# Optimization experiments

Measured on AMD Instinct MI355X. Metric: run time of the kernel, lower is better.

Reference implementation:

```python
import jax, jax.numpy as jnp
import numpy as np

B, T, D_IN, H, L, OUT, S = 128, 256, 8, 512, 2, 2, 32
A = H  # attention_size == hidden_size


def lstm_cell(h, c, xt, Wih, Whh, b):
    # PyTorch LSTM gate order: i, f, g, o ; b = b_ih + b_hh (combined)
    g = xt @ Wih.T + h @ Whh.T + b
    i, f, gg, o = jnp.split(g, 4, axis=-1)
    c = jax.nn.sigmoid(f) * c + jax.nn.sigmoid(i) * jnp.tanh(gg)
    h = jax.nn.sigmoid(o) * jnp.tanh(c)
    return h, c


def setup_inputs() -> dict:
    key = jax.random.key(0)
    ks = jax.random.split(key, 20)
    w = lambda k, shape: jax.random.normal(k, shape, jnp.float32) * 0.1
    return {
        "x": jax.random.normal(ks[0], (B, T, D_IN), jnp.float32),
        # bidirectional encoder, 2 layers; leading dim 2 = (fwd, bwd)
        "enc_Wih0": w(ks[1], (2, 4 * H, D_IN)),
        "enc_Whh0": w(ks[2], (2, 4 * H, H)),
        "enc_b0": w(ks[3], (2, 4 * H)),
        "enc_Wih1": w(ks[4], (2, 4 * H, 2 * H)),
        "enc_Whh1": w(ks[5], (2, 4 * H, H)),
        "enc_b1": w(ks[6], (2, 4 * H)),
        # unidirectional decoder, 2 layers; layer0 input = output_size + 2H
        "dec_Wih0": w(ks[7], (4 * H, 2 * H + OUT)),
        "dec_Whh0": w(ks[8], (4 * H, H)),
        "dec_b0": w(ks[9], (4 * H,)),
        "dec_Wih1": w(ks[10], (4 * H, H)),
        "dec_Whh1": w(ks[11], (4 * H, H)),
        "dec_b1": w(ks[12], (4 * H,)),
        # Bahdanau attention (no biases)
        "Wa": w(ks[13], (A, 2 * H)),
        "Ua": w(ks[14], (A, H)),
        "Va": w(ks[15], (1, A)),
        "proj_W": w(ks[16], (H, H)),
        "proj_b": jnp.zeros((H,), jnp.float32),
        "fc_W": w(ks[17], (OUT, H)),
        "fc_b": jnp.zeros((OUT,), jnp.float32),
    }


def _forward(x, enc_Wih0, enc_Whh0, enc_b0, enc_Wih1, enc_Whh1, enc_b1,
             dec_Wih0, dec_Whh0, dec_b0, dec_Wih1, dec_Whh1, dec_b1,
             Wa, Ua, Va, proj_W, proj_b, fc_W, fc_b):
    Bb = x.shape[0]
    xT = jnp.swapaxes(x, 0, 1)  # [T,B,D]

    def run_dir(seq, Wih, Whh, b, reverse):
        h0 = jnp.zeros((Bb, H), x.dtype)
        def step(carry, xt):
            h, c = lstm_cell(carry[0], carry[1], xt, Wih, Whh, b)
            return (h, c), h
        (hT, cT), hs = jax.lax.scan(step, (h0, h0), seq, reverse=reverse)
        return hs, hT, cT

    # encoder layer 0 (bidirectional)
    of, hf0, cf0 = run_dir(xT, enc_Wih0[0], enc_Whh0[0], enc_b0[0], False)
    ob, hb0, cb0 = run_dir(xT, enc_Wih0[1], enc_Whh0[1], enc_b0[1], True)
    l1in = jnp.concatenate([of, ob], -1)  # [T,B,2H]
    # encoder layer 1
    of1, hf1, cf1 = run_dir(l1in, enc_Wih1[0], enc_Whh1[0], enc_b1[0], False)
    ob1, hb1, cb1 = run_dir(l1in, enc_Wih1[1], enc_Whh1[1], enc_b1[1], True)
    enc_out = jnp.swapaxes(jnp.concatenate([of1, ob1], -1), 0, 1)  # [B,T,2H]

    # torch hidden order: [l0_fwd, l0_bwd, l1_fwd, l1_bwd]; code takes first num_layers=2
    dh = jnp.tanh(jnp.stack([hf0, hb0]) @ proj_W.T + proj_b)  # [2,B,H]
    dc = jnp.stack([cf0, cb0])

    Wa_vals = enc_out @ Wa.T  # [B,T,A], loop-invariant part of attention
    y0 = x[:, -1, :OUT]

    def dec_step(carry, _):
        h, c, y = carry
        q = h[-1]  # [B,H] last-layer hidden
        score = jnp.tanh(Wa_vals + (q @ Ua.T)[:, None, :]) @ Va.T  # [B,T,1]
        wts = jax.nn.softmax(score, axis=1)
        z = jnp.sum(wts * enc_out, axis=1)  # [B,2H]
        h0n, c0n = lstm_cell(h[0], c[0], jnp.concatenate([y, z], 1), dec_Wih0, dec_Whh0, dec_b0)
        h1n, c1n = lstm_cell(h[1], c[1], h0n, dec_Wih1, dec_Whh1, dec_b1)
        yn = h1n @ fc_W.T + fc_b  # [B,OUT]
        return (jnp.stack([h0n, h1n]), jnp.stack([c0n, c1n]), yn), yn

    _, ys = jax.lax.scan(dec_step, (dh, dc, y0), None, length=S)
    return jnp.swapaxes(ys, 0, 1)  # [B,S,OUT]


def reference(x, enc_Wih0, enc_Whh0, enc_b0, enc_Wih1, enc_Whh1, enc_b1,
              dec_Wih0, dec_Whh0, dec_b0, dec_Wih1, dec_Whh1, dec_b1,
              Wa, Ua, Va, proj_W, proj_b, fc_W, fc_b):
    return _forward(x, enc_Wih0, enc_Whh0, enc_b0, enc_Wih1, enc_Whh1, enc_b1,
                    dec_Wih0, dec_Whh0, dec_b0, dec_Wih1, dec_Whh1, dec_b1,
                    Wa, Ua, Va, proj_W, proj_b, fc_W, fc_b)
```

## Files before the change

kernel.cpp:

```cpp
#include <hip/hip_runtime.h>

typedef _Float16 h16;
typedef __attribute__((ext_vector_type(8))) _Float16 f16x8;
typedef __attribute__((ext_vector_type(4))) float f32x4;
typedef unsigned long long u64;
typedef unsigned int u32;
typedef unsigned short u16;

#define B_ 128
#define T_ 256
#define H_ 512
#define S_ 32
#define MFMA __builtin_amdgcn_mfma_f32_16x16x32_f16

__device__ __forceinline__ float fexp2(float x){ return __builtin_amdgcn_exp2f(x); }
__device__ __forceinline__ float frcp (float x){ return __builtin_amdgcn_rcpf(x); }
__device__ __forceinline__ float fsig (float x){ return frcp(1.f + fexp2(-1.44269504089f*x)); }
__device__ __forceinline__ float ftanh(float x){ return 1.f - 2.f*frcp(1.f + fexp2(2.88539008178f*x)); }

__device__ __forceinline__ f16x8 ld16_coh(const h16* p) {
  u64 q0 = __hip_atomic_load((const u64*)p,     __ATOMIC_RELAXED, __HIP_MEMORY_SCOPE_AGENT);
  u64 q1 = __hip_atomic_load((const u64*)p + 1, __ATOMIC_RELAXED, __HIP_MEMORY_SCOPE_AGENT);
  u64 a[2] = {q0, q1};
  f16x8 v; __builtin_memcpy(&v, a, 16);
  return v;
}
__device__ __forceinline__ float ld4f_coh(const float* p) {
  u32 b = __hip_atomic_load((const u32*)p, __ATOMIC_RELAXED, __HIP_MEMORY_SCOPE_AGENT);
  float v; __builtin_memcpy(&v, &b, 4);
  return v;
}
__device__ __forceinline__ float ld2h_coh(const h16* p) {
  u16 b = __hip_atomic_load((const u16*)p, __ATOMIC_RELAXED, __HIP_MEMORY_SCOPE_AGENT);
  h16 v; __builtin_memcpy(&v, &b, 2);
  return (float)v;
}
__device__ __forceinline__ void st2_coh(h16* p, h16 v) {
  u16 b; __builtin_memcpy(&b, &v, 2);
  __hip_atomic_store((u16*)p, b, __ATOMIC_RELAXED, __HIP_MEMORY_SCOPE_AGENT);
}
__device__ __forceinline__ void st4_coh(float* p, float v) {
  u32 b; __builtin_memcpy(&b, &v, 4);
  __hip_atomic_store((u32*)p, b, __ATOMIC_RELAXED, __HIP_MEMORY_SCOPE_AGENT);
}

__device__ __forceinline__ void gridbar(u32* slots, int myslot, int base,
                                        int n, u32 ep, int tid) {
  __syncthreads();
  if (tid == 0)
    __hip_atomic_store(&slots[(size_t)myslot * 32], ep, __ATOMIC_RELAXED, __HIP_MEMORY_SCOPE_AGENT);
  bool ok;
  do {
    ok = (tid < n) ? (__hip_atomic_load(&slots[(size_t)(base + tid) * 32],
                                        __ATOMIC_RELAXED, __HIP_MEMORY_SCOPE_AGENT) >= ep)
                   : true;
  } while (!__syncthreads_and(ok));
  __syncthreads();
}

struct EncP {
  const h16 *xpad, *Wih0, *Whh0, *Wih1, *Whh1;
  const float *b0, *b1;
  h16 *l1in, *encout;
  float *cdump;
  u32* slots;
};

__global__ __launch_bounds__(512, 1) void encoder_persist(EncP P) {
  const int wg = blockIdx.x, dir = wg >> 7;
  const int j0 = (wg & 127) << 2;
  const int tid = threadIdx.x, wid = tid >> 6, lane = tid & 63;
  const int col = lane & 15, rowg = lane >> 4;
  const int u = col & 3, gt = col >> 2;
  const int m0 = wid << 4;

  __shared__ h16 W[16][1544];

  auto stage = [&](const h16* Wih, int Kx, const h16* Whh) {
    const int CX = Kx >> 3, CT = CX + 64;
    for (int i = tid; i < 16 * CT; i += 512) {
      const int r = i / CT, c = i - r * CT;
      const int grow = (r >> 2) * 512 + j0 + (r & 3);
      f16x8 v = (c < CX) ? *(const f16x8*)(Wih + (size_t)grow * Kx + (c << 3))
                         : *(const f16x8*)(Whh + (size_t)grow * 512 + ((c - CX) << 3));
      *(f16x8*)(&W[r][c << 3]) = v;
    }
  };
  auto pick = [&](float own, float p4, float p8, float p12, int x) {
    return x == 0 ? own : x == 1 ? p4 : x == 2 ? p8 : p12;
  };

  u32 ep = 0;
  float c0_ = 0.f, c1_ = 0.f, c2_ = 0.f, c3_ = 0.f;
  float h0, h1, h2, h3;

#define GATECOMB(av_, cvar, hvar, bias_)                                        \
  { float a_ = av_ + bias_;                                                     \
    float p4_ = __shfl_xor(a_, 4), p8_ = __shfl_xor(a_, 8), p12_ = __shfl_xor(a_, 12); \
    float iv = pick(a_, p4_, p8_, p12_, gt);                                    \
    float fv = pick(a_, p4_, p8_, p12_, gt ^ 1);                                \
    float gv = pick(a_, p4_, p8_, p12_, gt ^ 2);                                \
    float ov = pick(a_, p4_, p8_, p12_, gt ^ 3);                                \
    cvar = fsig(fv) * cvar + fsig(iv) * ftanh(gv);                              \
    hvar = fsig(ov) * ftanh(cvar); }

  stage(P.Wih0 + (size_t)dir * 2048 * 32, 32, P.Whh0 + (size_t)dir * 2048 * 512);
  const float bias0 = P.b0[dir * 2048 + gt * 512 + j0 + u];
  __syncthreads();

  for (int i = 0; i < 256; ++i) {
    const int t = dir ? 255 - i : i;
    f32x4 acc = {0.f, 0.f, 0.f, 0.f};
    {
      f16x8 av = *(const f16x8*)(P.xpad + ((size_t)(m0 + col) * T_ + t) * 32 + rowg * 8);
      f16x8 bv = *(const f16x8*)(&W[col][rowg * 8]);
      acc = MFMA(av, bv, acc, 0, 0, 0);
    }
    if (i) {
      const int tp = dir ? t + 1 : t - 1;
      const h16* ah = P.l1in + ((size_t)tp * B_ + m0 + col) * 1024 + dir * 512 + rowg * 8;
      #pragma unroll
      for (int ks = 0; ks < 16; ++ks) {
        f16x8 av = ld16_coh(ah + ks * 32);
        f16x8 bv = *(const f16x8*)(&W[col][32 + ks * 32 + rowg * 8]);
        acc = MFMA(av, bv, acc, 0, 0, 0);
      }
    }
    GATECOMB(acc[0], c0_, h0, bias0) GATECOMB(acc[1], c1_, h1, bias0)
    GATECOMB(acc[2], c2_, h2, bias0) GATECOMB(acc[3], c3_, h3, bias0)
    const float hw = (gt == 0) ? h0 : (gt == 1) ? h1 : (gt == 2) ? h2 : h3;
    const int bm = m0 + (rowg << 2) + gt;
    st2_coh(&P.l1in[((size_t)t * B_ + bm) * 1024 + dir * 512 + j0 + u], (h16)hw);
    gridbar(P.slots, wg, dir << 7, 128, ++ep, tid);
  }
  {
    const float cw = (gt == 0) ? c0_ : (gt == 1) ? c1_ : (gt == 2) ? c2_ : c3_;
    const int bm = m0 + (rowg << 2) + gt;
    P.cdump[(size_t)dir * B_ * H_ + (size_t)bm * H_ + j0 + u] = cw;
  }
  gridbar(P.slots, wg, 0, 256, ++ep, tid);

  stage(P.Wih1 + (size_t)dir * 2048 * 1024, 1024, P.Whh1 + (size_t)dir * 2048 * 512);
  const float bias1 = P.b1[dir * 2048 + gt * 512 + j0 + u];
  c0_ = c1_ = c2_ = c3_ = 0.f;
  __syncthreads();

  for (int i = 0; i < 256; ++i) {
    const int t = dir ? 255 - i : i;
    f32x4 acc = {0.f, 0.f, 0.f, 0.f};
    const h16* ax = P.l1in + ((size_t)t * B_ + m0 + col) * 1024 + rowg * 8;
    #pragma unroll
    for (int ks = 0; ks < 32; ++ks) {
      f16x8 av = *(const f16x8*)(ax + ks * 32);
      f16x8 bv = *(const f16x8*)(&W[col][ks * 32 + rowg * 8]);
      acc = MFMA(av, bv, acc, 0, 0, 0);
    }
    if (i) {
      const int tp = dir ? t + 1 : t - 1;
      const h16* ah = P.encout + ((size_t)(m0 + col) * T_ + tp) * 1024 + dir * 512 + rowg * 8;
      #pragma unroll
      for (int ks = 0; ks < 16; ++ks) {
        f16x8 av = ld16_coh(ah + ks * 32);
        f16x8 bv = *(const f16x8*)(&W[col][1024 + ks * 32 + rowg * 8]);
        acc = MFMA(av, bv, acc, 0, 0, 0);
      }
    }
    GATECOMB(acc[0], c0_, h0, bias1) GATECOMB(acc[1], c1_, h1, bias1)
    GATECOMB(acc[2], c2_, h2, bias1) GATECOMB(acc[3], c3_, h3, bias1)
    const float hw = (gt == 0) ? h0 : (gt == 1) ? h1 : (gt == 2) ? h2 : h3;
    const int bm = m0 + (rowg << 2) + gt;
    st2_coh(&P.encout[((size_t)bm * T_ + t) * 1024 + dir * 512 + j0 + u], (h16)hw);
    gridbar(P.slots, wg, dir << 7, 128, ++ep, tid);
  }
#undef GATECOMB
}

struct DecP {
  const h16 *bUa, *WaV, *enc, *bdWih0, *bdWhh0, *bdWih1, *bdWhh1;
  const float *Va, *db0, *db1, *fcW, *fcb, *cdump;
  float *qUa, *score, *out;
  h16 *xcat, *dh0, *dh1;
  u32* slots;
};

__global__ __launch_bounds__(512, 1) void decoder_persist(DecP D) {
  const int wg = blockIdx.x, tid = threadIdx.x;
  const int wid = tid >> 6, lane = tid & 63;
  const int col = lane & 15, rowg = lane >> 4;
  const int gw = wg * 8 + wid;
  const int mt = wg >> 5, ut = wg & 31;
  const int mi = tid >> 4, ji = tid & 15;

  __shared__ h16 Ast[16][1576];
  __shared__ float gtl[4][16][16];
  __shared__ float sred[256], swts[256];

  float c0r = 0.f, c1r = 0.f;
  if (tid < 256) {
    c0r = D.cdump[(size_t)(mt * 16 + mi) * 512 + ut * 16 + ji];
    c1r = D.cdump[(size_t)B_ * H_ + (size_t)(mt * 16 + mi) * 512 + ut * 16 + ji];
  }
  u32 ep = 0;

  for (int s = 0; s < S_; ++s) {
    const int par = s & 1;
    const h16* h1c = D.dh1 + (size_t)par * B_ * H_;
    h16* h1n = D.dh1 + (size_t)(par ^ 1) * B_ * H_;
    const h16* h0c = D.dh0 + (size_t)par * B_ * H_;
    h16* h0n = D.dh0 + (size_t)(par ^ 1) * B_ * H_;

    if (gw < 256) {
      const int qmt = gw >> 5, qnt = gw & 31;
      f32x4 acc = {0, 0, 0, 0};
      const h16* ap = h1c + (size_t)(qmt * 16 + col) * 512 + rowg * 8;
      const h16* bp = D.bUa + (size_t)(qnt * 16 + col) * 512 + rowg * 8;
      #pragma unroll
      for (int kc = 0; kc < 16; ++kc) {
        f16x8 av = ld16_coh(ap + kc * 32);
        f16x8 bv = *(const f16x8*)(bp + kc * 32);
        acc = MFMA(av, bv, acc, 0, 0, 0);
      }
      #pragma unroll
      for (int t2 = 0; t2 < 4; ++t2)
        st4_coh(D.qUa + (size_t)(qmt * 16 + rowg * 4 + t2) * 512 + qnt * 16 + col, acc[t2]);
    } else if (gw < 512 && s > 0) {
      const int idx = gw - 256, m = idx >> 1, o = idx & 1;
      float sum = 0.f;
      #pragma unroll
      for (int i2 = 0; i2 < 8; ++i2) {
        const int k = i2 * 64 + lane;
        sum += ld2h_coh(h1c + (size_t)m * 512 + k) * D.fcW[o * 512 + k];
      }
      #pragma unroll
      for (int o2 = 32; o2; o2 >>= 1) sum += __shfl_xor(sum, o2);
      if (lane == 0) {
        const float y = sum + D.fcb[o];
        D.out[(size_t)m * (S_ * 2) + (s - 1) * 2 + o] = y;
        st2_coh(D.xcat + (size_t)m * 1056 + o, (h16)y);
      }
    }
    gridbar(D.slots, wg, 0, 256, ++ep, tid);

    {
      const int m = gw >> 4, tg = gw & 15;
      float q[8], va[8];
      #pragma unroll
      for (int i2 = 0; i2 < 8; ++i2) {
        q[i2] = ld4f_coh(D.qUa + (size_t)m * 512 + i2 * 64 + lane);
        va[i2] = D.Va[i2 * 64 + lane];
      }
      for (int tt = 0; tt < 16; ++tt) {
        const int t = tg * 16 + tt;
        const h16* wrow = D.WaV + ((size_t)m * 256 + t) * 512;
        float ssum = 0.f;
        #pragma unroll
        for (int i2 = 0; i2 < 8; ++i2)
          ssum += ftanh((float)wrow[i2 * 64 + lane] + q[i2]) * va[i2];
        #pragma unroll
        for (int o2 = 32; o2; o2 >>= 1) ssum += __shfl_xor(ssum, o2);
        if (lane == 0) st4_coh(D.score + (size_t)m * 256 + t, ssum);
      }
    }
    gridbar(D.slots, wg, 0, 256, ++ep, tid);

    if (wg < 128) {
      const int m = wg;
      const float sv = (tid < 256) ? ld4f_coh(D.score + (size_t)m * 256 + tid) : -1e30f;
      if (tid < 256) sred[tid] = sv;
      __syncthreads();
      for (int o2 = 128; o2; o2 >>= 1) { if (tid < o2) sred[tid] = fmaxf(sred[tid], sred[tid + o2]); __syncthreads(); }
      const float mx = sred[0]; __syncthreads();
      const float p = (tid < 256) ? fexp2((sv - mx) * 1.44269504089f) : 0.f;
      if (tid < 256) sred[tid] = p;
      __syncthreads();
      for (int o2 = 128; o2; o2 >>= 1) { if (tid < o2) sred[tid] += sred[tid + o2]; __syncthreads(); }
      if (tid < 256) swts[tid] = p * frcp(sred[0]);
      __syncthreads();
      const h16* erow = D.enc + (size_t)m * 256 * 1024;
      #pragma unroll
      for (int half = 0; half < 2; ++half) {
        const int k = tid + half * 512;
        float a0 = 0, a1 = 0, a2 = 0, a3 = 0;
        for (int t = 0; t < 256; t += 4) {
          a0 += swts[t    ] * (float)erow[(t    ) * 1024 + k];
          a1 += swts[t + 1] * (float)erow[(t + 1) * 1024 + k];
          a2 += swts[t + 2] * (float)erow[(t + 2) * 1024 + k];
          a3 += swts[t + 3] * (float)erow[(t + 3) * 1024 + k];
        }
        st2_coh(D.xcat + (size_t)m * 1056 + 2 + k, (h16)((a0 + a1) + (a2 + a3)));
      }
    }
    gridbar(D.slots, wg, 0, 256, ++ep, tid);

    {
      for (int i2 = tid; i2 < 16 * 196; i2 += 512) {
        const int r = i2 / 196, c = i2 - r * 196;
        f16x8 v = (c < 132) ? ld16_coh(D.xcat + (size_t)(mt * 16 + r) * 1056 + c * 8)
                            : ld16_coh(h0c + (size_t)(mt * 16 + r) * 512 + (c - 132) * 8);
        *(f16x8*)&Ast[r][c * 8] = v;
      }
      __syncthreads();
      if (wid < 4) {
        const int n = wid * 512 + ut * 16 + col;
        f32x4 acc = {0, 0, 0, 0};
        const h16* w1 = D.bdWih0 + (size_t)n * 1056 + rowg * 8;
        const h16* w2 = D.bdWhh0 + (size_t)n * 512 + rowg * 8;
        #pragma unroll
        for (int kc = 0; kc < 33; ++kc) {
          f16x8 av = *(const f16x8*)&Ast[col][kc * 32 + rowg * 8];
          f16x8 bv = *(const f16x8*)(w1 + kc * 32);
          acc = MFMA(av, bv, acc, 0, 0, 0);
        }
        #pragma unroll
        for (int kc = 0; kc < 16; ++kc) {
          f16x8 av = *(const f16x8*)&Ast[col][1056 + kc * 32 + rowg * 8];
          f16x8 bv = *(const f16x8*)(w2 + kc * 32);
          acc = MFMA(av, bv, acc, 0, 0, 0);
        }
        #pragma unroll
        for (int t2 = 0; t2 < 4; ++t2) gtl[wid][rowg * 4 + t2][col] = acc[t2];
      }
      __syncthreads();
      if (tid < 256) {
        const int jj = ut * 16 + ji;
        const float iv = gtl[0][mi][ji] + D.db0[jj];
        const float fv = gtl[1][mi][ji] + D.db0[512 + jj];
        const float gv = gtl[2][mi][ji] + D.db0[1024 + jj];
        const float ov = gtl[3][mi][ji] + D.db0[1536 + jj];
        c0r = fsig(fv) * c0r + fsig(iv) * ftanh(gv);
        st2_coh(h0n + (size_t)(mt * 16 + mi) * 512 + jj, (h16)(fsig(ov) * ftanh(c0r)));
      }
    }
    gridbar(D.slots, wg, 0, 256, ++ep, tid);

    {
      for (int i2 = tid; i2 < 16 * 128; i2 += 512) {
        const int r = i2 >> 7, c = i2 & 127;
        f16x8 v = (c < 64) ? ld16_coh(h0n + (size_t)(mt * 16 + r) * 512 + c * 8)
                           : ld16_coh(h1c + (size_t)(mt * 16 + r) * 512 + (c - 64) * 8);
        *(f16x8*)&Ast[r][c * 8] = v;
      }
      __syncthreads();
      if (wid < 4) {
        const int n = wid * 512 + ut * 16 + col;
        f32x4 acc = {0, 0, 0, 0};
        const h16* w1 = D.bdWih1 + (size_t)n * 512 + rowg * 8;
        const h16* w2 = D.bdWhh1 + (size_t)n * 512 + rowg * 8;
        #pragma unroll
        for (int kc = 0; kc < 16; ++kc) {
          f16x8 av = *(const f16x8*)&Ast[col][kc * 32 + rowg * 8];
          f16x8 bv = *(const f16x8*)(w1 + kc * 32);
          acc = MFMA(av, bv, acc, 0, 0, 0);
        }
        #pragma unroll
        for (int kc = 0; kc < 16; ++kc) {
          f16x8 av = *(const f16x8*)&Ast[col][512 + kc * 32 + rowg * 8];
          f16x8 bv = *(const f16x8*)(w2 + kc * 32);
          acc = MFMA(av, bv, acc, 0, 0, 0);
        }
        #pragma unroll
        for (int t2 = 0; t2 < 4; ++t2) gtl[wid][rowg * 4 + t2][col] = acc[t2];
      }
      __syncthreads();
      if (tid < 256) {
        const int jj = ut * 16 + ji;
        const float iv = gtl[0][mi][ji] + D.db1[jj];
        const float fv = gtl[1][mi][ji] + D.db1[512 + jj];
        const float gv = gtl[2][mi][ji] + D.db1[1024 + jj];
        const float ov = gtl[3][mi][ji] + D.db1[1536 + jj];
        c1r = fsig(fv) * c1r + fsig(iv) * ftanh(gv);
        st2_coh(h1n + (size_t)(mt * 16 + mi) * 512 + jj, (h16)(fsig(ov) * ftanh(c1r)));
      }
    }
    gridbar(D.slots, wg, 0, 256, ++ep, tid);
  }

  if (gw < 256) {
    const int m = gw >> 1, o = gw & 1;
    const h16* h1f = D.dh1;
    float sum = 0.f;
    #pragma unroll
    for (int i2 = 0; i2 < 8; ++i2) {
      const int k = i2 * 64 + lane;
      sum += ld2h_coh(h1f + (size_t)m * 512 + k) * D.fcW[o * 512 + k];
    }
    #pragma unroll
    for (int o2 = 32; o2; o2 >>= 1) sum += __shfl_xor(sum, o2);
    if (lane == 0) D.out[(size_t)m * (S_ * 2) + (S_ - 1) * 2 + o] = sum + D.fcb[o];
  }
}

__global__ __launch_bounds__(256) void gemm_tn(const h16* Am, int lda, const h16* Bm,
                                               const float* bias, void* Cout, int ldc,
                                               int K, int mode) {
  const int wid = threadIdx.x >> 6, lane = threadIdx.x & 63;
  const int r = lane & 15, g = lane >> 4;
  const int m0 = (blockIdx.x * 4 + wid) * 16;
  const int n0 = blockIdx.y * 64;
  f32x4 acc[4] = {{0,0,0,0},{0,0,0,0},{0,0,0,0},{0,0,0,0}};
  const h16* ap = Am + (size_t)(m0 + r) * lda + g * 8;
  const h16* bp = Bm + (size_t)(n0 + r) * K + g * 8;
  for (int k = 0; k < K; k += 32) {
    f16x8 av = *(const f16x8*)(ap + k);
    #pragma unroll
    for (int j = 0; j < 4; ++j) {
      f16x8 bv = *(const f16x8*)(bp + (size_t)j * 16 * K + k);
      acc[j] = MFMA(av, bv, acc[j], 0, 0, 0);
    }
  }
  #pragma unroll
  for (int j = 0; j < 4; ++j) {
    const int n = n0 + j * 16 + r;
    const float badd = bias ? bias[n] : 0.f;
    #pragma unroll
    for (int t = 0; t < 4; ++t) {
      const int m = m0 + g * 4 + t;
      float v = acc[j][t] + badd;
      if (mode == 2) v = ftanh(v);
      if (mode == 0) ((float*)Cout)[(size_t)m * ldc + n] = v;
      else           ((h16*)Cout) [(size_t)m * ldc + n] = (h16)v;
    }
  }
}

__global__ void convert_pad(const float* __restrict__ in, h16* __restrict__ out,
                            int rows, int Kin, int Kout) {
  const size_t i = (size_t)blockIdx.x * 256 + threadIdx.x;
  if (i >= (size_t)rows * Kout) return;
  const int r = (int)(i / Kout), k = (int)(i % Kout);
  out[i] = (k < Kin) ? (h16)in[(size_t)r * Kin + k] : (h16)0.f;
}

__global__ void y0_init(const float* __restrict__ x, h16* __restrict__ xcat) {
  const int tid = threadIdx.x;
  if (tid < 256) {
    const int m = tid >> 1, o = tid & 1;
    xcat[(size_t)m * 1056 + o] = (h16)x[(size_t)(m * T_ + (T_ - 1)) * 8 + o];
  }
}

extern "C" void kernel_launch(void* const* d_in, const int* in_sizes, int n_in,
                              void* d_out, int out_size, void* d_ws, size_t ws_size,
                              hipStream_t stream) {
  const float* x     = (const float*)d_in[0];
  const float* eWih0 = (const float*)d_in[1];
  const float* eWhh0 = (const float*)d_in[2];
  const float* eb0   = (const float*)d_in[3];
  const float* eWih1 = (const float*)d_in[4];
  const float* eWhh1 = (const float*)d_in[5];
  const float* eb1   = (const float*)d_in[6];
  const float* dWih0 = (const float*)d_in[7];
  const float* dWhh0 = (const float*)d_in[8];
  const float* db0   = (const float*)d_in[9];
  const float* dWih1 = (const float*)d_in[10];
  const float* dWhh1 = (const float*)d_in[11];
  const float* db1   = (const float*)d_in[12];
  const float* Wa    = (const float*)d_in[13];
  const float* Ua    = (const float*)d_in[14];
  const float* Va    = (const float*)d_in[15];
  const float* projW = (const float*)d_in[16];
  const float* projb = (const float*)d_in[17];
  const float* fcW   = (const float*)d_in[18];
  const float* fcb   = (const float*)d_in[19];
  float* out = (float*)d_out;

  size_t cur = 0;
  auto alloc = [&](size_t bytes) {
    void* p = (char*)d_ws + cur;
    cur += (bytes + 255) & ~(size_t)255;
    return p;
  };
  h16*  xpad   = (h16*) alloc((size_t)B_ * T_ * 32 * 2);
  h16*  l1in   = (h16*) alloc((size_t)T_ * B_ * 1024 * 2);
  h16*  encout = (h16*) alloc((size_t)B_ * T_ * 1024 * 2);
  h16*  WaV    = (h16*) alloc((size_t)B_ * T_ * H_ * 2);
  float* cdump = (float*)alloc((size_t)2 * B_ * H_ * 4);
  float* score = (float*)alloc((size_t)B_ * T_ * 4);
  float* qUa   = (float*)alloc((size_t)B_ * H_ * 4);
  h16*  xcat   = (h16*) alloc((size_t)B_ * 1056 * 2);
  h16*  dh0    = (h16*) alloc((size_t)2 * B_ * H_ * 2);
  h16*  dh1    = (h16*) alloc((size_t)2 * B_ * H_ * 2);
  u32*  slots  = (u32*) alloc((size_t)2 * 256 * 32 * 4);
  h16*  bWih0  = (h16*) alloc((size_t)2 * 2048 * 32 * 2);
  h16*  bWhh0  = (h16*) alloc((size_t)2 * 2048 * 512 * 2);
  h16*  bWih1  = (h16*) alloc((size_t)2 * 2048 * 1024 * 2);
  h16*  bWhh1  = (h16*) alloc((size_t)2 * 2048 * 512 * 2);
  h16*  bdWih0 = (h16*) alloc((size_t)2048 * 1056 * 2);
  h16*  bdWhh0 = (h16*) alloc((size_t)2048 * 512 * 2);
  h16*  bdWih1 = (h16*) alloc((size_t)2048 * 512 * 2);
  h16*  bdWhh1 = (h16*) alloc((size_t)2048 * 512 * 2);
  h16*  bWa    = (h16*) alloc((size_t)512 * 1024 * 2);
  h16*  bUa    = (h16*) alloc((size_t)512 * 512 * 2);
  h16*  bprojW = (h16*) alloc((size_t)512 * 512 * 2);
  if (cur > ws_size) return;

  (void)hipMemsetAsync(slots, 0, (size_t)2 * 256 * 32 * 4, stream);
  (void)hipMemsetAsync(xcat, 0, (size_t)B_ * 1056 * 2, stream);

  auto conv = [&](const float* in, h16* o, int rows, int kin, int kout) {
    const size_t total = (size_t)rows * kout;
    convert_pad<<<dim3((unsigned)((total + 255) / 256)), dim3(256), 0, stream>>>(in, o, rows, kin, kout);
  };
  conv(x,     xpad,   B_ * T_,  8,    32);
  conv(eWih0, bWih0,  2 * 2048, 8,    32);
  conv(eWhh0, bWhh0,  2 * 2048, 512,  512);
  conv(eWih1, bWih1,  2 * 2048, 1024, 1024);
  conv(eWhh1, bWhh1,  2 * 2048, 512,  512);
  conv(dWih0, bdWih0, 2048,     1026, 1056);
  conv(dWhh0, bdWhh0, 2048,     512,  512);
  conv(dWih1, bdWih1, 2048,     512,  512);
  conv(dWhh1, bdWhh1, 2048,     512,  512);
  conv(Wa,    bWa,    512,      1024, 1024);
  conv(Ua,    bUa,    512,      512,  512);
  conv(projW, bprojW, 512,      512,  512);

  EncP P;
  P.xpad = xpad; P.Wih0 = bWih0; P.Whh0 = bWhh0; P.Wih1 = bWih1; P.Whh1 = bWhh1;
  P.b0 = eb0; P.b1 = eb1; P.l1in = l1in; P.encout = encout; P.cdump = cdump; P.slots = slots;
  encoder_persist<<<dim3(256), dim3(512), 0, stream>>>(P);

  gemm_tn<<<dim3(B_ * T_ / 64, 8), dim3(256), 0, stream>>>(encout, 1024, bWa, nullptr, WaV, 512, 1024, 1);
  gemm_tn<<<dim3(B_ / 64, 8), dim3(256), 0, stream>>>(l1in + (size_t)(T_ - 1) * B_ * 1024, 1024,
                                                      bprojW, projb, dh0, 512, 512, 2);
  gemm_tn<<<dim3(B_ / 64, 8), dim3(256), 0, stream>>>(l1in + 512, 1024,
                                                      bprojW, projb, dh1, 512, 512, 2);
  y0_init<<<dim3(1), dim3(256), 0, stream>>>(x, xcat);

  DecP D;
  D.bUa = bUa; D.WaV = WaV; D.enc = encout;
  D.bdWih0 = bdWih0; D.bdWhh0 = bdWhh0; D.bdWih1 = bdWih1; D.bdWhh1 = bdWhh1;
  D.Va = Va; D.db0 = db0; D.db1 = db1; D.fcW = fcW; D.fcb = fcb; D.cdump = cdump;
  D.qUa = qUa; D.score = score; D.out = out;
  D.xcat = xcat; D.dh0 = dh0; D.dh1 = dh1;
  D.slots = slots + 256 * 32;
  decoder_persist<<<dim3(256), dim3(512), 0, stream>>>(D);
}
```

Baseline: 10.75 ms.

## Replace epoch-slot grid barriers with per-step atomic counters and prefetch input projection

```diff
diff --git a/kernel.cpp b/kernel.cpp
--- a/kernel.cpp
+++ b/kernel.cpp
@@ -13,6 +13,13 @@
 #define S_ 32
 #define MFMA __builtin_amdgcn_mfma_f32_16x16x32_f16
 
+#define SLOT_L0F 0
+#define SLOT_L0B 257
+#define SLOT_ALL 514
+#define SLOT_L1F 515
+#define SLOT_L1B 771
+#define SLOT_DEC 1027
+
 __device__ __forceinline__ float fexp2(float x){ return __builtin_amdgcn_exp2f(x); }
 __device__ __forceinline__ float frcp (float x){ return __builtin_amdgcn_rcpf(x); }
 __device__ __forceinline__ float fsig (float x){ return frcp(1.f + fexp2(-1.44269504089f*x)); }
@@ -44,18 +51,13 @@
   __hip_atomic_store((u32*)p, b, __ATOMIC_RELAXED, __HIP_MEMORY_SCOPE_AGENT);
 }
 
-__device__ __forceinline__ void gridbar(u32* slots, int myslot, int base,
-                                        int n, u32 ep, int tid) {
+__device__ __forceinline__ void bar_arrive(u32* c, int tid) {
   __syncthreads();
-  if (tid == 0)
-    __hip_atomic_store(&slots[(size_t)myslot * 32], ep, __ATOMIC_RELAXED, __HIP_MEMORY_SCOPE_AGENT);
-  bool ok;
-  do {
-    ok = (tid < n) ? (__hip_atomic_load(&slots[(size_t)(base + tid) * 32],
-                                        __ATOMIC_RELAXED, __HIP_MEMORY_SCOPE_AGENT) >= ep)
-                   : true;
-  } while (!__syncthreads_and(ok));
-  __syncthreads();
+  if (tid == 0) atomicAdd(c, 1u);
+}
+__device__ __forceinline__ void bar_wait(const u32* c, u32 n) {
+  while (__hip_atomic_load(c, __ATOMIC_RELAXED, __HIP_MEMORY_SCOPE_AGENT) < n) {}
+  __builtin_amdgcn_sched_barrier(0);
 }
 
 struct EncP {
@@ -63,7 +65,7 @@
   const float *b0, *b1;
   h16 *l1in, *encout;
   float *cdump;
-  u32* slots;
+  u32* cnt;
 };
 
 __global__ __launch_bounds__(512, 1) void encoder_persist(EncP P) {
@@ -89,8 +91,28 @@
   auto pick = [&](float own, float p4, float p8, float p12, int x) {
     return x == 0 ? own : x == 1 ? p4 : x == 2 ? p8 : p12;
   };
-
-  u32 ep = 0;
+  auto xpart0 = [&](int t) -> f32x4 {
+    f32x4 a = {0.f, 0.f, 0.f, 0.f};
+    f16x8 av = *(const f16x8*)(P.xpad + ((size_t)(m0 + col) * T_ + t) * 32 + rowg * 8);
+    f16x8 bv = *(const f16x8*)(&W[col][rowg * 8]);
+    return MFMA(av, bv, a, 0, 0, 0);
+  };
+  auto xpart1 = [&](int t) -> f32x4 {
+    f32x4 a = {0.f, 0.f, 0.f, 0.f};
+    const h16* ax = P.l1in + ((size_t)t * B_ + m0 + col) * 1024 + rowg * 8;
+    #pragma unroll
+    for (int ks = 0; ks < 32; ++ks) {
+      f16x8 av = *(const f16x8*)(ax + ks * 32);
+      f16x8 bv = *(const f16x8*)(&W[col][ks * 32 + rowg * 8]);
+      a = MFMA(av, bv, a, 0, 0, 0);
+    }
+    return a;
+  };
+
+  u32* cL0 = P.cnt + (size_t)(dir ? SLOT_L0B : SLOT_L0F) * 16;
+  u32* cL1 = P.cnt + (size_t)(dir ? SLOT_L1B : SLOT_L1F) * 16;
+  u32* cAll = P.cnt + (size_t)SLOT_ALL * 16;
+
   float c0_ = 0.f, c1_ = 0.f, c2_ = 0.f, c3_ = 0.f;
   float h0, h1, h2, h3;
 
@@ -108,15 +130,12 @@
   const float bias0 = P.b0[dir * 2048 + gt * 512 + j0 + u];
   __syncthreads();
 
+  f32x4 accx = xpart0(dir ? 255 : 0);
   for (int i = 0; i < 256; ++i) {
     const int t = dir ? 255 - i : i;
-    f32x4 acc = {0.f, 0.f, 0.f, 0.f};
-    {
-      f16x8 av = *(const f16x8*)(P.xpad + ((size_t)(m0 + col) * T_ + t) * 32 + rowg * 8);
-      f16x8 bv = *(const f16x8*)(&W[col][rowg * 8]);
-      acc = MFMA(av, bv, acc, 0, 0, 0);
-    }
+    f32x4 acc = accx;
     if (i) {
+      bar_wait(cL0 + (size_t)(i - 1) * 16, 128);
       const int tp = dir ? t + 1 : t - 1;
       const h16* ah = P.l1in + ((size_t)tp * B_ + m0 + col) * 1024 + dir * 512 + rowg * 8;
       #pragma unroll
@@ -131,31 +150,28 @@
     const float hw = (gt == 0) ? h0 : (gt == 1) ? h1 : (gt == 2) ? h2 : h3;
     const int bm = m0 + (rowg << 2) + gt;
     st2_coh(&P.l1in[((size_t)t * B_ + bm) * 1024 + dir * 512 + j0 + u], (h16)hw);
-    gridbar(P.slots, wg, dir << 7, 128, ++ep, tid);
+    bar_arrive(cL0 + (size_t)i * 16, tid);
+    if (i < 255) accx = xpart0(dir ? 254 - i : i + 1);
   }
   {
     const float cw = (gt == 0) ? c0_ : (gt == 1) ? c1_ : (gt == 2) ? c2_ : c3_;
     const int bm = m0 + (rowg << 2) + gt;
     P.cdump[(size_t)dir * B_ * H_ + (size_t)bm * H_ + j0 + u] = cw;
   }
-  gridbar(P.slots, wg, 0, 256, ++ep, tid);
+  bar_arrive(cAll, tid);
+  bar_wait(cAll, 256);
 
   stage(P.Wih1 + (size_t)dir * 2048 * 1024, 1024, P.Whh1 + (size_t)dir * 2048 * 512);
   const float bias1 = P.b1[dir * 2048 + gt * 512 + j0 + u];
   c0_ = c1_ = c2_ = c3_ = 0.f;
   __syncthreads();
 
+  accx = xpart1(dir ? 255 : 0);
   for (int i = 0; i < 256; ++i) {
     const int t = dir ? 255 - i : i;
-    f32x4 acc = {0.f, 0.f, 0.f, 0.f};
-    const h16* ax = P.l1in + ((size_t)t * B_ + m0 + col) * 1024 + rowg * 8;
-    #pragma unroll
-    for (int ks = 0; ks < 32; ++ks) {
-      f16x8 av = *(const f16x8*)(ax + ks * 32);
-      f16x8 bv = *(const f16x8*)(&W[col][ks * 32 + rowg * 8]);
-      acc = MFMA(av, bv, acc, 0, 0, 0);
-    }
+    f32x4 acc = accx;
     if (i) {
+      bar_wait(cL1 + (size_t)(i - 1) * 16, 128);
       const int tp = dir ? t + 1 : t - 1;
       const h16* ah = P.encout + ((size_t)(m0 + col) * T_ + tp) * 1024 + dir * 512 + rowg * 8;
       #pragma unroll
@@ -170,7 +186,8 @@
     const float hw = (gt == 0) ? h0 : (gt == 1) ? h1 : (gt == 2) ? h2 : h3;
     const int bm = m0 + (rowg << 2) + gt;
     st2_coh(&P.encout[((size_t)bm * T_ + t) * 1024 + dir * 512 + j0 + u], (h16)hw);
-    gridbar(P.slots, wg, dir << 7, 128, ++ep, tid);
+    bar_arrive(cL1 + (size_t)i * 16, tid);
+    if (i < 255) accx = xpart1(dir ? 254 - i : i + 1);
   }
 #undef GATECOMB
 }
@@ -180,7 +197,7 @@
   const float *Va, *db0, *db1, *fcW, *fcb, *cdump;
   float *qUa, *score, *out;
   h16 *xcat, *dh0, *dh1;
-  u32* slots;
+  u32* cnt;
 };
 
 __global__ __launch_bounds__(512, 1) void decoder_persist(DecP D) {
@@ -195,12 +212,19 @@
   __shared__ float gtl[4][16][16];
   __shared__ float sred[256], swts[256];
 
+  u32* cD = D.cnt + (size_t)SLOT_DEC * 16;
+  u32 ep = 0;
+  auto dbar = [&]() {
+    bar_arrive(cD + (size_t)ep * 16, tid);
+    bar_wait(cD + (size_t)ep * 16, 256);
+    ++ep;
+  };
+
   float c0r = 0.f, c1r = 0.f;
   if (tid < 256) {
     c0r = D.cdump[(size_t)(mt * 16 + mi) * 512 + ut * 16 + ji];
     c1r = D.cdump[(size_t)B_ * H_ + (size_t)(mt * 16 + mi) * 512 + ut * 16 + ji];
   }
-  u32 ep = 0;
 
   for (int s = 0; s < S_; ++s) {
     const int par = s & 1;
@@ -239,7 +263,7 @@
         st2_coh(D.xcat + (size_t)m * 1056 + o, (h16)y);
       }
     }
-    gridbar(D.slots, wg, 0, 256, ++ep, tid);
+    dbar();
 
     {
       const int m = gw >> 4, tg = gw & 15;
@@ -261,7 +285,7 @@
         if (lane == 0) st4_coh(D.score + (size_t)m * 256 + t, ssum);
       }
     }
-    gridbar(D.slots, wg, 0, 256, ++ep, tid);
+    dbar();
 
     if (wg < 128) {
       const int m = wg;
@@ -290,7 +314,7 @@
         st2_coh(D.xcat + (size_t)m * 1056 + 2 + k, (h16)((a0 + a1) + (a2 + a3)));
       }
     }
-    gridbar(D.slots, wg, 0, 256, ++ep, tid);
+    dbar();
 
     {
       for (int i2 = tid; i2 < 16 * 196; i2 += 512) {
@@ -331,7 +355,7 @@
         st2_coh(h0n + (size_t)(mt * 16 + mi) * 512 + jj, (h16)(fsig(ov) * ftanh(c0r)));
       }
     }
-    gridbar(D.slots, wg, 0, 256, ++ep, tid);
+    dbar();
 
     {
       for (int i2 = tid; i2 < 16 * 128; i2 += 512) {
@@ -372,7 +396,7 @@
         st2_coh(h1n + (size_t)(mt * 16 + mi) * 512 + jj, (h16)(fsig(ov) * ftanh(c1r)));
       }
     }
-    gridbar(D.slots, wg, 0, 256, ++ep, tid);
+    dbar();
   }
 
   if (gw < 256) {
@@ -480,7 +504,7 @@
   h16*  xcat   = (h16*) alloc((size_t)B_ * 1056 * 2);
   h16*  dh0    = (h16*) alloc((size_t)2 * B_ * H_ * 2);
   h16*  dh1    = (h16*) alloc((size_t)2 * B_ * H_ * 2);
-  u32*  slots  = (u32*) alloc((size_t)2 * 256 * 32 * 4);
+  u32*  cnt    = (u32*) alloc((size_t)2048 * 16 * 4);
   h16*  bWih0  = (h16*) alloc((size_t)2 * 2048 * 32 * 2);
   h16*  bWhh0  = (h16*) alloc((size_t)2 * 2048 * 512 * 2);
   h16*  bWih1  = (h16*) alloc((size_t)2 * 2048 * 1024 * 2);
@@ -494,7 +518,7 @@
   h16*  bprojW = (h16*) alloc((size_t)512 * 512 * 2);
   if (cur > ws_size) return;
 
-  (void)hipMemsetAsync(slots, 0, (size_t)2 * 256 * 32 * 4, stream);
+  (void)hipMemsetAsync(cnt, 0, (size_t)2048 * 16 * 4, stream);
   (void)hipMemsetAsync(xcat, 0, (size_t)B_ * 1056 * 2, stream);
 
   auto conv = [&](const float* in, h16* o, int rows, int kin, int kout) {
@@ -516,7 +540,7 @@
 
   EncP P;
   P.xpad = xpad; P.Wih0 = bWih0; P.Whh0 = bWhh0; P.Wih1 = bWih1; P.Whh1 = bWhh1;
-  P.b0 = eb0; P.b1 = eb1; P.l1in = l1in; P.encout = encout; P.cdump = cdump; P.slots = slots;
+  P.b0 = eb0; P.b1 = eb1; P.l1in = l1in; P.encout = encout; P.cdump = cdump; P.cnt = cnt;
   encoder_persist<<<dim3(256), dim3(512), 0, stream>>>(P);
 
   gemm_tn<<<dim3(B_ * T_ / 64, 8), dim3(256), 0, stream>>>(encout, 1024, bWa, nullptr, WaV, 512, 1024, 1);
@@ -532,6 +556,6 @@
   D.Va = Va; D.db0 = db0; D.db1 = db1; D.fcW = fcW; D.fcb = fcb; D.cdump = cdump;
   D.qUa = qUa; D.score = score; D.out = out;
   D.xcat = xcat; D.dh0 = dh0; D.dh1 = dh1;
-  D.slots = slots + 256 * 32;
+  D.cnt = cnt;
   decoder_persist<<<dim3(256), dim3(512), 0, stream>>>(D);
 }
```

Result: slower. 12.43 ms (+15.6%).
